# Kernel optimization log

Hardware: AMD Instinct MI355X
Metric: run time of the kernel (lower is better)

Reference implementation:

```python
import jax, jax.numpy as jnp
import numpy as np

DIM = 2048
N_HEADS = 32
N_KV = 8
HEAD_DIM = DIM // N_HEADS  # 64
N_REP = N_HEADS // N_KV    # 4
HALF = HEAD_DIM // 2
B = 2
T = 2048
THETA = 10000.0


def _rope(x, cos, sin):
    # x: [B,H,T,hd]; cos/sin: [T,HALF]. Pairs are interleaved (..., half, 2),
    # matching torch.view_as_complex on a (..., -1, 2) reshape.
    xr = x.reshape(x.shape[:-1] + (HALF, 2))
    x0, x1 = xr[..., 0], xr[..., 1]
    o0 = x0 * cos - x1 * sin
    o1 = x0 * sin + x1 * cos
    return jnp.stack([o0, o1], axis=-1).reshape(x.shape)


def setup_inputs() -> dict:
    key = jax.random.key(0)
    ks = jax.random.split(key, 6)
    x = jax.random.normal(ks[0], (B, T, DIM), dtype=jnp.float32)
    scale = 0.02
    wq = jax.random.normal(ks[1], (N_HEADS * HEAD_DIM, DIM), dtype=jnp.float32) * scale
    wk = jax.random.normal(ks[2], (N_KV * HEAD_DIM, DIM), dtype=jnp.float32) * scale
    wv = jax.random.normal(ks[3], (N_KV * HEAD_DIM, DIM), dtype=jnp.float32) * scale
    wo = jax.random.normal(ks[4], (DIM, DIM), dtype=jnp.float32) * scale
    # causal mask [1,1,T,T]
    mask = jnp.tril(jnp.ones((T, T), dtype=jnp.int32))[None, None]
    # RoPE tables (precompute_freqs_cis with theta=10000, scaling_factor=1.0)
    freqs = 1.0 / THETA ** (jnp.arange(HALF, dtype=jnp.float32) / HALF)
    angles = jnp.arange(2 * T, dtype=jnp.float32)[:, None] * freqs[None, :]
    return {"x": x, "mask": mask, "wq": wq, "wk": wk, "wv": wv, "wo": wo,
            "cos": jnp.cos(angles), "sin": jnp.sin(angles)}


def reference(x, mask, wq, wk, wv, wo, cos, sin):
    Bx, Tx, C = x.shape
    q = (x @ wq.T).reshape(Bx, Tx, N_HEADS, HEAD_DIM).transpose(0, 2, 1, 3)
    k = (x @ wk.T).reshape(Bx, Tx, N_KV, HEAD_DIM).transpose(0, 2, 1, 3)
    v = (x @ wv.T).reshape(Bx, Tx, N_KV, HEAD_DIM).transpose(0, 2, 1, 3)
    q = _rope(q, cos[:Tx], sin[:Tx])
    k = _rope(k, cos[:Tx], sin[:Tx])
    # GQA: head h attends to kv head h // N_REP (repeat_interleave semantics)
    qg = q.reshape(Bx, N_KV, N_REP, Tx, HEAD_DIM)
    att = jnp.einsum('bgrtd,bgsd->bgrts', qg, k) * (HEAD_DIM ** -0.5)
    m = mask[0, 0, :Tx, :Tx]  # broadcast over b,g,r
    att = jnp.where(m == 0, -jnp.inf, att)
    att = jax.nn.softmax(att, axis=-1)
    og = jnp.einsum('bgrts,bgsd->bgrtd', att, v)
    out = og.reshape(Bx, N_HEADS, Tx, HEAD_DIM).transpose(0, 2, 1, 3).reshape(Bx, Tx, C)
    return out @ wo.T
```

## Files before the change

### kernel.cpp

```cpp
#include <hip/hip_runtime.h>
#include <hip/hip_bf16.h>

typedef unsigned short u16;
typedef __attribute__((ext_vector_type(8))) short s16x8;
typedef __attribute__((ext_vector_type(4))) float f32x4;
typedef __attribute__((ext_vector_type(16))) float f32x16;
typedef __attribute__((ext_vector_type(4))) float f32x4v;
typedef __attribute__((ext_vector_type(4))) u16 u16x4;

#define DIM 2048
#define NH 32
#define NKV 8
#define HD 64
#define TT 2048
#define BB 2
#define MT (BB * TT)

__device__ __forceinline__ u16 f2bf(float f) {
    union { float f; unsigned u; } v; v.f = f;
    unsigned r = v.u + 0x7FFFu + ((v.u >> 16) & 1u);
    return (u16)(r >> 16);
}
__device__ __forceinline__ float bf2f(u16 h) {
    union { unsigned u; float f; } v; v.u = ((unsigned)h) << 16;
    return v.f;
}
__device__ __forceinline__ u16 cvtbf(float f) {
    __hip_bfloat16 hb = __float2bfloat16(f);
    return *reinterpret_cast<u16*>(&hb);
}
__device__ __forceinline__ void plane32swap(unsigned& a, unsigned& b) {
#if defined(__has_builtin)
#if __has_builtin(__builtin_amdgcn_permlane32_swap)
    auto t = __builtin_amdgcn_permlane32_swap((int)a, (int)b, false, false);
    a = (unsigned)t[0]; b = (unsigned)t[1];
#else
    asm volatile("v_permlane32_swap_b32 %0, %1" : "+v"(a), "+v"(b));
#endif
#else
    asm volatile("v_permlane32_swap_b32 %0, %1" : "+v"(a), "+v"(b));
#endif
}

__global__ void k_convert_all(const float* __restrict__ x, const float* __restrict__ wq,
                              const float* __restrict__ wk, const float* __restrict__ wv,
                              const float* __restrict__ wo,
                              u16* __restrict__ xb, u16* __restrict__ wqkv, u16* __restrict__ wob) {
    long i = (long)(blockIdx.x * 256 + threadIdx.x) * 4;
    const float* src; u16* dst; long o = i;
    if (o < 8388608L)            { src = x;  dst = xb; }
    else if ((o -= 8388608L) < 4194304L) { src = wq; dst = wqkv; }
    else if ((o -= 4194304L) < 1048576L) { src = wk; dst = wqkv + 4194304L; }
    else if ((o -= 1048576L) < 1048576L) { src = wv; dst = wqkv + 5242880L; }
    else { o -= 1048576L;          src = wo; dst = wob; }
    f32x4v f = *(const f32x4v*)(src + o);
    u16x4 out;
    #pragma unroll
    for (int e = 0; e < 4; ++e) out[e] = f2bf(f[e]);
    *(u16x4*)(dst + o) = out;
}

template<int BNF, bool OUTF32>
__global__ __launch_bounds__(512, 2) void k_gemm256(const u16* __restrict__ A, const u16* __restrict__ B,
                                                    void* __restrict__ C, int M, int N, int K) {
    constexpr int BN = 64 * BNF;
    constexpr int BH = 2048 * BNF;
    __shared__ u16 LDS[32768 + 4 * BH];
    const int nTn = N / BN;
    const int nwg = gridDim.x;
    const int wg = (blockIdx.x & 7) * (nwg >> 3) + (blockIdx.x >> 3);
    const int tm = wg / nTn, tn = wg % nTn;
    const int tid = threadIdx.x, wid = tid >> 6, lane = tid & 63;
    const int wr = wid >> 2, wc = wid & 3;
    const u16* Ab = A + (size_t)tm * 256 * K;
    const u16* Bb = B + (size_t)tn * BN * K;

    f32x4 acc[8][BNF] = {};
    s16x8 af[4], bfr[BNF];

    auto STAGE_A = [&](int buf, int kk, int kt) {
        u16* base = LDS + (buf * 2 + kk) * 8192;
        const u16* g = Ab + kt * 64 + kk * 32;
        #pragma unroll
        for (int i = 0; i < 2; ++i) {
            const int s = i * 512 + tid;
            const int row = s >> 2;
            const int cl = (s & 3) ^ ((row >> 1) & 3);
            __builtin_amdgcn_global_load_lds(
                (const __attribute__((address_space(1))) void*)(g + (size_t)row * K + cl * 8),
                (__attribute__((address_space(3))) void*)(base + (i * 512 + wid * 64) * 8), 16, 0, 0);
        }
    };
    auto STAGE_B = [&](int buf, int kk, int kt) {
        u16* base = LDS + 32768 + (buf * 2 + kk) * BH;
        const u16* g = Bb + kt * 64 + kk * 32;
        auto one = [&](int ch) {
            const int row = ch * 16 + (lane >> 2);
            const int cl = (lane & 3) ^ ((row >> 1) & 3);
            __builtin_amdgcn_global_load_lds(
                (const __attribute__((address_space(1))) void*)(g + (size_t)row * K + cl * 8),
                (__attribute__((address_space(3))) void*)(base + ch * 512), 16, 0, 0);
        };
        if constexpr (BNF == 4) { one(wid); one(8 + wid); }
        else if constexpr (BNF == 3) { one(wid); one(8 + (wid & 3)); }
        else { one(wid); }
    };
    auto LDA = [&](int buf, int kk, int mh) {
        const u16* base = LDS + (buf * 2 + kk) * 8192;
        #pragma unroll
        for (int m2 = 0; m2 < 4; ++m2) {
            const int row = wr * 128 + (mh * 4 + m2) * 16 + (lane & 15);
            const int cl = (lane >> 4) ^ ((row >> 1) & 3);
            af[m2] = *(const s16x8*)(base + row * 32 + cl * 8);
        }
    };
    auto LDB = [&](int buf, int kk) {
        const u16* base = LDS + 32768 + (buf * 2 + kk) * BH;
        #pragma unroll
        for (int n = 0; n < BNF; ++n) {
            const int row = wc * (16 * BNF) + n * 16 + (lane & 15);
            const int cl = (lane >> 4) ^ ((row >> 1) & 3);
            bfr[n] = *(const s16x8*)(base + row * 32 + cl * 8);
        }
    };
    auto MFMA16 = [&](int mh) {
        asm volatile("s_waitcnt lgkmcnt(0)" ::: "memory");
        __builtin_amdgcn_sched_barrier(0);
        __builtin_amdgcn_s_setprio(1);
        #pragma unroll
        for (int m2 = 0; m2 < 4; ++m2)
            #pragma unroll
            for (int n = 0; n < BNF; ++n)
                acc[mh * 4 + m2][n] =
                    __builtin_amdgcn_mfma_f32_16x16x32_bf16(af[m2], bfr[n], acc[mh * 4 + m2][n], 0, 0, 0);
        __builtin_amdgcn_s_setprio(0);
    };

    #define VMID() do { if constexpr (BNF == 2) asm volatile("s_waitcnt vmcnt(6)" ::: "memory"); \
                        else                    asm volatile("s_waitcnt vmcnt(8)" ::: "memory"); } while (0)
    #define VONE() do { if constexpr (BNF == 2) asm volatile("s_waitcnt vmcnt(3)" ::: "memory"); \
                        else                    asm volatile("s_waitcnt vmcnt(4)" ::: "memory"); } while (0)

    STAGE_A(0, 0, 0); STAGE_B(0, 0, 0);
    STAGE_A(0, 1, 0); STAGE_B(0, 1, 0);
    STAGE_A(1, 0, 1); STAGE_B(1, 0, 1);
    VMID();
    __builtin_amdgcn_s_barrier();

    const int NI = K >> 7;
    for (int it = 0; it < NI; ++it) {
        const bool last = (it == NI - 1);
        const int t1 = 2 * it + 1;
        LDA(0, 0, 0); LDB(0, 0);
        STAGE_A(1, 1, t1);
        __builtin_amdgcn_s_barrier();
        MFMA16(0);
        __builtin_amdgcn_s_barrier();

        LDA(0, 0, 1);
        STAGE_B(1, 1, t1);
        __builtin_amdgcn_s_barrier();
        MFMA16(1);
        VMID();
        __builtin_amdgcn_s_barrier();

        LDA(0, 1, 0); LDB(0, 1);
        if (!last) STAGE_A(0, 0, t1 + 1);
        __builtin_amdgcn_s_barrier();
        MFMA16(0);
        __builtin_amdgcn_s_barrier();

        LDA(0, 1, 1);
        if (!last) STAGE_B(0, 0, t1 + 1);
        __builtin_amdgcn_s_barrier();
        MFMA16(1);
        if (!last) VMID(); else VONE();
        __builtin_amdgcn_s_barrier();

        LDA(1, 0, 0); LDB(1, 0);
        if (!last) STAGE_A(0, 1, t1 + 1);
        __builtin_amdgcn_s_barrier();
        MFMA16(0);
        __builtin_amdgcn_s_barrier();

        LDA(1, 0, 1);
        if (!last) STAGE_B(0, 1, t1 + 1);
        __builtin_amdgcn_s_barrier();
        MFMA16(1);
        if (!last) VMID(); else asm volatile("s_waitcnt vmcnt(0)" ::: "memory");
        __builtin_amdgcn_s_barrier();

        LDA(1, 1, 0); LDB(1, 1);
        if (!last) STAGE_A(1, 0, t1 + 2);
        __builtin_amdgcn_s_barrier();
        MFMA16(0);
        __builtin_amdgcn_s_barrier();

        LDA(1, 1, 1);
        if (!last) STAGE_B(1, 0, t1 + 2);
        __builtin_amdgcn_s_barrier();
        MFMA16(1);
        if (!last) VMID();
        __builtin_amdgcn_s_barrier();
    }
    #undef VMID
    #undef VONE

    #pragma unroll
    for (int mf = 0; mf < 8; ++mf)
        #pragma unroll
        for (int n = 0; n < BNF; ++n)
            #pragma unroll
            for (int r = 0; r < 4; ++r) {
                const int row = tm * 256 + wr * 128 + mf * 16 + (lane >> 4) * 4 + r;
                const int col = tn * BN + wc * (16 * BNF) + n * 16 + (lane & 15);
                if (OUTF32) ((float*)C)[(size_t)row * N + col] = acc[mf][n][r];
                else        ((u16*)C)[(size_t)row * N + col] = f2bf(acc[mf][n][r]);
            }
}

__global__ void k_rope(const u16* __restrict__ qkv, const float* __restrict__ ct, const float* __restrict__ st,
                       u16* __restrict__ qo, u16* __restrict__ ko, u16* __restrict__ vo) {
    const int idx = blockIdx.x * 256 + threadIdx.x;
    const int c = idx % 384;
    const int bt = idx / 384;
    const int b = bt / TT, t = bt % TT;
    const s16x8 v = *(const s16x8*)(qkv + (size_t)bt * 3072 + c * 8);
    if (c < 320) {
        const bool isq = c < 256;
        const int base = isq ? c : c - 256;
        const int hh = base >> 3;
        const int di0 = (base & 7) * 4;
        const f32x4v cc = *(const f32x4v*)(ct + t * 32 + di0);
        const f32x4v ss = *(const f32x4v*)(st + t * 32 + di0);
        const float QS = isq ? 0.18033688f : 1.0f;
        s16x8 o;
        #pragma unroll
        for (int p = 0; p < 4; ++p) {
            const float x0 = bf2f((u16)v[2 * p]), x1 = bf2f((u16)v[2 * p + 1]);
            o[2 * p]     = (short)cvtbf((x0 * cc[p] - x1 * ss[p]) * QS);
            o[2 * p + 1] = (short)cvtbf((x0 * ss[p] + x1 * cc[p]) * QS);
        }
        u16* dst = isq ? (qo + ((size_t)(b * NH + hh) * TT + t) * HD + 2 * di0)
                       : (ko + ((size_t)(b * NKV + hh) * TT + t) * HD + 2 * di0);
        *(s16x8*)dst = o;
    } else {
        const int base = c - 320;
        const int hh = base >> 3;
        const int d0 = (base & 7) * 8;
        *(s16x8*)(vo + ((size_t)(b * NKV + hh) * TT + t) * HD + d0) = v;
    }
}

__global__ __launch_bounds__(256) void k_vtrans(const u16* __restrict__ vp, u16* __restrict__ vt) {
    __shared__ u16 tile[64][66];
    const int bg = blockIdx.x >> 5;
    const int t0 = (blockIdx.x & 31) * 64;
    const int tid = threadIdx.x;
    #pragma unroll
    for (int c = 0; c < 2; ++c) {
        const int idx = c * 256 + tid;
        const int tl = idx >> 3, dc = idx & 7;
        s16x8 v = *(const s16x8*)(vp + ((size_t)bg * TT + t0 + tl) * HD + dc * 8);
        *(s16x8*)(&tile[tl][dc * 8]) = v;
    }
    __syncthreads();
    #pragma unroll
    for (int c = 0; c < 2; ++c) {
        const int idx = c * 256 + tid;
        const int d = idx >> 3, tc = idx & 7;
        s16x8 v;
        #pragma unroll
        for (int e = 0; e < 8; ++e) v[e] = (short)tile[tc * 8 + e][d];
        *(s16x8*)(vt + ((size_t)bg * HD + d) * TT + t0 + tc * 8) = v;
    }
}

__global__ __launch_bounds__(512) void k_attn(const u16* __restrict__ Q, const u16* __restrict__ K,
                                              const u16* __restrict__ Vtg, u16* __restrict__ O) {
    const int bid = blockIdx.x;
    const int gq = bid >> 6;
    const int qt8 = (gq < 4) ? (7 - gq) : (gq - 4);
    const int bh = bid & 63;
    const int h = bh & 31;
    const int b = bh >> 5;
    const int g = h >> 2;
    __shared__ u16 Ks[3][4096];
    __shared__ u16 Vs[3][4096];
    const int tid = threadIdx.x, wave = tid >> 6, lane = tid & 63;
    const int c = lane & 31, hi = lane >> 5;
    const u16* Qg = Q + ((size_t)(b * NH + h) * TT + qt8 * 256) * HD;
    const u16* Kg = K + (size_t)(b * NKV + g) * TT * HD;
    const u16* Vg = Vtg + (size_t)(b * NKV + g) * HD * TT;

    s16x8 qa[4];
    #pragma unroll
    for (int kb = 0; kb < 4; ++kb)
        qa[kb] = *(const s16x8*)(Qg + (size_t)(wave * 32 + c) * HD + kb * 16 + hi * 8);

    const int rl = lane >> 3, ccl = lane & 7;
    const int sc = ccl ^ rl;
    auto stage = [&](int jj, int bi) {
        const int r = wave * 8 + rl;
        __builtin_amdgcn_global_load_lds(
            (const __attribute__((address_space(1))) void*)(Kg + ((size_t)(jj * 64 + r)) * HD + sc * 8),
            (__attribute__((address_space(3))) void*)(Ks[bi] + wave * 512), 16, 0, 0);
        __builtin_amdgcn_global_load_lds(
            (const __attribute__((address_space(1))) void*)(Vg + (size_t)r * TT + jj * 64 + sc * 8),
            (__attribute__((address_space(3))) void*)(Vs[bi] + wave * 512), 16, 0, 0);
    };

    f32x16 acc0 = {}, acc1 = {};
    float l = 0.f;
    const int ntiles = 4 * qt8 + 4;

    stage(0, 0);
    stage(1, 1);

    for (int j = 0; j < ntiles; ++j) {
        if (j < ntiles - 1) asm volatile("s_waitcnt vmcnt(2)" ::: "memory");
        else                asm volatile("s_waitcnt vmcnt(0)" ::: "memory");
        __builtin_amdgcn_s_barrier();
        if (j + 2 < ntiles) stage(j + 2, (j + 2) % 3);
        const u16* Kb = Ks[j % 3];
        const u16* Vb = Vs[j % 3];

        f32x16 s0 = {}, s1 = {};
        __builtin_amdgcn_s_setprio(1);
        #pragma unroll
        for (int kb = 0; kb < 4; ++kb) {
            const s16x8 kf0 = *(const s16x8*)(Kb + c * 64 + (((2 * kb + hi) ^ ccl) * 8));
            const s16x8 kf1 = *(const s16x8*)(Kb + (32 + c) * 64 + (((2 * kb + hi) ^ ccl) * 8));
            s0 = __builtin_amdgcn_mfma_f32_32x32x16_bf16(kf0, qa[kb], s0, 0, 0, 0);
            s1 = __builtin_amdgcn_mfma_f32_32x32x16_bf16(kf1, qa[kb], s1, 0, 0, 0);
        }
        __builtin_amdgcn_s_setprio(0);

        if (j >= ntiles - 4) {
            const int kb64 = (j - (ntiles - 4)) * 64;
            if (kb64 + 63 > wave * 32) {
                const int q_loc = wave * 32 + c;
                #pragma unroll
                for (int r = 0; r < 16; ++r) {
                    const int crow = (r & 3) + 8 * (r >> 2) + 4 * hi;
                    if (kb64 + crow > q_loc)      s0[r] = -1e30f;
                    if (kb64 + 32 + crow > q_loc) s1[r] = -1e30f;
                }
            }
        }
        float tsum[4] = {0.f, 0.f, 0.f, 0.f};
        #pragma unroll
        for (int r = 0; r < 16; ++r) {
            s0[r] = __builtin_amdgcn_exp2f(s0[r]); tsum[r & 3] += s0[r];
            s1[r] = __builtin_amdgcn_exp2f(s1[r]); tsum[r & 3] += s1[r];
        }
        l += (tsum[0] + tsum[1]) + (tsum[2] + tsum[3]);

        unsigned W0[8], W1[8];
        #pragma unroll
        for (int m = 0; m < 8; ++m) {
            float a0f = s0[2 * m], a1f = s0[2 * m + 1];
            float b0f = s1[2 * m], b1f = s1[2 * m + 1];
            asm("v_cvt_pk_bf16_f32 %0, %1, %2" : "=v"(W0[m]) : "v"(a0f), "v"(a1f));
            asm("v_cvt_pk_bf16_f32 %0, %1, %2" : "=v"(W1[m]) : "v"(b0f), "v"(b1f));
        }
        s16x8 pa[4];
        #pragma unroll
        for (int ks = 0; ks < 4; ++ks) {
            const int base = 4 * (ks & 1);
            unsigned a0 = (ks < 2) ? W0[base + 0] : W1[base + 0];
            unsigned b0 = (ks < 2) ? W0[base + 2] : W1[base + 2];
            unsigned a1 = (ks < 2) ? W0[base + 1] : W1[base + 1];
            unsigned b1 = (ks < 2) ? W0[base + 3] : W1[base + 3];
            plane32swap(a0, b0);
            plane32swap(a1, b1);
            union { unsigned w[4]; s16x8 v; } u;
            u.w[0] = a0; u.w[1] = a1; u.w[2] = b0; u.w[3] = b1;
            pa[ks] = u.v;
        }

        __builtin_amdgcn_s_setprio(1);
        #pragma unroll
        for (int kb = 0; kb < 4; ++kb) {
            const s16x8 vb0 = *(const s16x8*)(Vb + c * 64 + (((2 * kb + hi) ^ ccl) * 8));
            const s16x8 vb1 = *(const s16x8*)(Vb + (32 + c) * 64 + (((2 * kb + hi) ^ ccl) * 8));
            acc0 = __builtin_amdgcn_mfma_f32_32x32x16_bf16(pa[kb], vb0, acc0, 0, 0, 0);
            acc1 = __builtin_amdgcn_mfma_f32_32x32x16_bf16(pa[kb], vb1, acc1, 0, 0, 0);
        }
        __builtin_amdgcn_s_setprio(0);
    }

    l += __shfl_xor(l, 32, 64);
    const float inv = 1.0f / l;
    #pragma unroll
    for (int r = 0; r < 16; ++r) {
        const int crow = (r & 3) + 8 * (r >> 2) + 4 * hi;
        const float li = __shfl(inv, crow, 64);
        const size_t row = (size_t)b * TT + qt8 * 256 + wave * 32 + crow;
        O[row * DIM + h * 64 + c]      = cvtbf(acc0[r] * li);
        O[row * DIM + h * 64 + 32 + c] = cvtbf(acc1[r] * li);
    }
}

extern "C" void kernel_launch(void* const* d_in, const int* in_sizes, int n_in,
                              void* d_out, int out_size, void* d_ws, size_t ws_size,
                              hipStream_t stream) {
    const float* x  = (const float*)d_in[0];
    const float* wq = (const float*)d_in[2];
    const float* wk = (const float*)d_in[3];
    const float* wv = (const float*)d_in[4];
    const float* wo = (const float*)d_in[5];
    const float* ct = (const float*)d_in[6];
    const float* st = (const float*)d_in[7];
    char* ws = (char*)d_ws;
    u16* xb   = (u16*)(ws);
    u16* wqkv = (u16*)(ws + 16777216);
    u16* wob  = (u16*)(ws + 29360128);
    u16* qkv  = (u16*)(ws + 37748736);
    u16* kr   = (u16*)(ws + 62914560);
    u16* vp   = (u16*)(ws + 67108864);
    u16* qr   = xb;
    u16* ao   = qkv;
    u16* vt   = wqkv;

    k_convert_all<<<18432, 256, 0, stream>>>(x, wq, wk, wv, wo, xb, wqkv, wob);

    k_gemm256<3, false><<<(MT / 256) * (3072 / 192), 512, 0, stream>>>(xb, wqkv, qkv, MT, 3072, DIM);
    k_rope<<<MT * 384 / 256, 256, 0, stream>>>(qkv, ct, st, qr, kr, vp);
    k_vtrans<<<BB * NKV * (TT / 64), 256, 0, stream>>>(vp, vt);
    k_attn<<<8 * 64, 512, 0, stream>>>(qr, kr, vt, ao);
    k_gemm256<2, true><<<(MT / 256) * (DIM / 128), 512, 0, stream>>>(ao, wob, d_out, MT, DIM, DIM);
}
```

Measured before the change: 171.8 us.

## Software-pipeline QK^T of next tile with softmax and PV of current tile

Restructures the attention loop so the QK^T MFMAs for tile j+1 are issued before the exp/convert/PV work for tile j, using ping-pong score registers and a two-way unrolled loop. The goal is to overlap MFMA latency with the VALU softmax work. The wait before each barrier is now a full vmcnt(0) instead of vmcnt(2), which may stall on the prefetch issued one iteration earlier. Launch bounds now also request a minimum occupancy, and the extra score registers add register pressure.

```diff
diff --git a/kernel.cpp b/kernel.cpp
--- a/kernel.cpp
+++ b/kernel.cpp
@@ -276,8 +276,8 @@
     }
 }
 
-__global__ __launch_bounds__(512) void k_attn(const u16* __restrict__ Q, const u16* __restrict__ K,
-                                              const u16* __restrict__ Vtg, u16* __restrict__ O) {
+__global__ __launch_bounds__(512, 4) void k_attn(const u16* __restrict__ Q, const u16* __restrict__ K,
+                                                 const u16* __restrict__ Vtg, u16* __restrict__ O) {
     const int bid = blockIdx.x;
     const int gq = bid >> 6;
     const int qt8 = (gq < 4) ? (7 - gq) : (gq - 4);
@@ -313,54 +313,48 @@
     f32x16 acc0 = {}, acc1 = {};
     float l = 0.f;
     const int ntiles = 4 * qt8 + 4;
-
-    stage(0, 0);
-    stage(1, 1);
-
-    for (int j = 0; j < ntiles; ++j) {
-        if (j < ntiles - 1) asm volatile("s_waitcnt vmcnt(2)" ::: "memory");
-        else                asm volatile("s_waitcnt vmcnt(0)" ::: "memory");
+    const int q_loc = wave * 32 + c;
+
+    auto body = [&](int j, f32x16& i0, f32x16& i1, f32x16& o0, f32x16& o1) {
+        asm volatile("s_waitcnt vmcnt(0)" ::: "memory");
         __builtin_amdgcn_s_barrier();
         if (j + 2 < ntiles) stage(j + 2, (j + 2) % 3);
-        const u16* Kb = Ks[j % 3];
-        const u16* Vb = Vs[j % 3];
-
-        f32x16 s0 = {}, s1 = {};
-        __builtin_amdgcn_s_setprio(1);
-        #pragma unroll
-        for (int kb = 0; kb < 4; ++kb) {
-            const s16x8 kf0 = *(const s16x8*)(Kb + c * 64 + (((2 * kb + hi) ^ ccl) * 8));
-            const s16x8 kf1 = *(const s16x8*)(Kb + (32 + c) * 64 + (((2 * kb + hi) ^ ccl) * 8));
-            s0 = __builtin_amdgcn_mfma_f32_32x32x16_bf16(kf0, qa[kb], s0, 0, 0, 0);
-            s1 = __builtin_amdgcn_mfma_f32_32x32x16_bf16(kf1, qa[kb], s1, 0, 0, 0);
-        }
-        __builtin_amdgcn_s_setprio(0);
+
+        o0 = f32x16{}; o1 = f32x16{};
+        if (j + 1 < ntiles) {
+            const u16* Kb = Ks[(j + 1) % 3];
+            __builtin_amdgcn_s_setprio(1);
+            #pragma unroll
+            for (int kb = 0; kb < 4; ++kb) {
+                const s16x8 kf0 = *(const s16x8*)(Kb + c * 64 + (((2 * kb + hi) ^ ccl) * 8));
+                const s16x8 kf1 = *(const s16x8*)(Kb + (32 + c) * 64 + (((2 * kb + hi) ^ ccl) * 8));
+                o0 = __builtin_amdgcn_mfma_f32_32x32x16_bf16(kf0, qa[kb], o0, 0, 0, 0);
+                o1 = __builtin_amdgcn_mfma_f32_32x32x16_bf16(kf1, qa[kb], o1, 0, 0, 0);
+            }
+            __builtin_amdgcn_s_setprio(0);
+        }
 
         if (j >= ntiles - 4) {
             const int kb64 = (j - (ntiles - 4)) * 64;
             if (kb64 + 63 > wave * 32) {
-                const int q_loc = wave * 32 + c;
                 #pragma unroll
                 for (int r = 0; r < 16; ++r) {
                     const int crow = (r & 3) + 8 * (r >> 2) + 4 * hi;
-                    if (kb64 + crow > q_loc)      s0[r] = -1e30f;
-                    if (kb64 + 32 + crow > q_loc) s1[r] = -1e30f;
+                    if (kb64 + crow > q_loc)      i0[r] = -1e30f;
+                    if (kb64 + 32 + crow > q_loc) i1[r] = -1e30f;
                 }
             }
         }
-        float tsum[4] = {0.f, 0.f, 0.f, 0.f};
         #pragma unroll
         for (int r = 0; r < 16; ++r) {
-            s0[r] = __builtin_amdgcn_exp2f(s0[r]); tsum[r & 3] += s0[r];
-            s1[r] = __builtin_amdgcn_exp2f(s1[r]); tsum[r & 3] += s1[r];
-        }
-        l += (tsum[0] + tsum[1]) + (tsum[2] + tsum[3]);
-
+            i0[r] = __builtin_amdgcn_exp2f(i0[r]); l += i0[r];
+            i1[r] = __builtin_amdgcn_exp2f(i1[r]); l += i1[r];
+        }
         unsigned W0[8], W1[8];
         #pragma unroll
         for (int m = 0; m < 8; ++m) {
-            float a0f = s0[2 * m], a1f = s0[2 * m + 1];
-            float b0f = s1[2 * m], b1f = s1[2 * m + 1];
+            float a0f = i0[2 * m], a1f = i0[2 * m + 1];
+            float b0f = i1[2 * m], b1f = i1[2 * m + 1];
             asm("v_cvt_pk_bf16_f32 %0, %1, %2" : "=v"(W0[m]) : "v"(a0f), "v"(a1f));
             asm("v_cvt_pk_bf16_f32 %0, %1, %2" : "=v"(W1[m]) : "v"(b0f), "v"(b1f));
         }
@@ -379,6 +373,7 @@
             pa[ks] = u.v;
         }
 
+        const u16* Vb = Vs[j % 3];
         __builtin_amdgcn_s_setprio(1);
         #pragma unroll
         for (int kb = 0; kb < 4; ++kb) {
@@ -388,6 +383,30 @@
             acc1 = __builtin_amdgcn_mfma_f32_32x32x16_bf16(pa[kb], vb1, acc1, 0, 0, 0);
         }
         __builtin_amdgcn_s_setprio(0);
+    };
+
+    stage(0, 0);
+    stage(1, 1);
+    f32x16 sA0, sA1, sB0, sB1;
+    asm volatile("s_waitcnt vmcnt(2)" ::: "memory");
+    __builtin_amdgcn_s_barrier();
+    sA0 = f32x16{}; sA1 = f32x16{};
+    {
+        const u16* Kb = Ks[0];
+        __builtin_amdgcn_s_setprio(1);
+        #pragma unroll
+        for (int kb = 0; kb < 4; ++kb) {
+            const s16x8 kf0 = *(const s16x8*)(Kb + c * 64 + (((2 * kb + hi) ^ ccl) * 8));
+            const s16x8 kf1 = *(const s16x8*)(Kb + (32 + c) * 64 + (((2 * kb + hi) ^ ccl) * 8));
+            sA0 = __builtin_amdgcn_mfma_f32_32x32x16_bf16(kf0, qa[kb], sA0, 0, 0, 0);
+            sA1 = __builtin_amdgcn_mfma_f32_32x32x16_bf16(kf1, qa[kb], sA1, 0, 0, 0);
+        }
+        __builtin_amdgcn_s_setprio(0);
+    }
+
+    for (int j = 0; j < ntiles; j += 2) {
+        body(j,     sA0, sA1, sB0, sB1);
+        body(j + 1, sB0, sB1, sA0, sA1);
     }
 
     l += __shfl_xor(l, 32, 64);
```

New measurement: 331.0 us. +92.7%, slower.
